# Optimization experiments

Measured on AMD Instinct MI355X. Metric: run time of the kernel, lower is better.

The kernel has to match this reference:

```python
import jax, jax.numpy as jnp
import numpy as np

N = 100000   # nodes
E = 1200000  # edges
D = 64       # emb_dim
XIN = 18     # x_dim + node_dim
XD = 16      # x_dim (output)
ED = 1       # edge_dim
L = 4        # num message-passing layers
G = 8        # graphs in batch (for global_mean_pool)


def setup_inputs() -> dict:
    key = jax.random.key(0)
    ks = iter(jax.random.split(key, 64))
    def nrm(shape, s=0.05):
        return jax.random.normal(next(ks), shape, dtype=jnp.float32) * s
    inp = {}
    inp["x"] = jax.random.normal(next(ks), (N, XIN), dtype=jnp.float32)
    inp["edge_attr"] = jax.random.normal(next(ks), (E, ED), dtype=jnp.float32)
    inp["W_in"] = nrm((XIN, D)); inp["b_in"] = jnp.zeros((D,), jnp.float32)
    # per-layer stacked params (leading dim L)
    inp["msg_W1"] = nrm((L, 2 * D + ED, D)); inp["msg_b1"] = jnp.zeros((L, D), jnp.float32)
    inp["msg_g1"] = jnp.ones((L, D), jnp.float32); inp["msg_be1"] = jnp.zeros((L, D), jnp.float32)
    inp["msg_W2"] = nrm((L, D, D)); inp["msg_b2"] = jnp.zeros((L, D), jnp.float32)
    inp["msg_g2"] = jnp.ones((L, D), jnp.float32); inp["msg_be2"] = jnp.zeros((L, D), jnp.float32)
    inp["upd_W1"] = nrm((L, 2 * D, D)); inp["upd_b1"] = jnp.zeros((L, D), jnp.float32)
    inp["upd_g1"] = jnp.ones((L, D), jnp.float32); inp["upd_be1"] = jnp.zeros((L, D), jnp.float32)
    inp["upd_W2"] = nrm((L, D, D)); inp["upd_b2"] = jnp.zeros((L, D), jnp.float32)
    inp["upd_g2"] = jnp.ones((L, D), jnp.float32); inp["upd_be2"] = jnp.zeros((L, D), jnp.float32)
    inp["reward_W"] = nrm((D, D)); inp["reward_b"] = jnp.zeros((D,), jnp.float32)
    inp["rout_W"] = nrm((D, 1)); inp["rout_b"] = jnp.zeros((1,), jnp.float32)
    inp["pred_W"] = nrm((D, D)); inp["pred_b"] = jnp.zeros((D,), jnp.float32)
    inp["pout_W"] = nrm((D, XD)); inp["pout_b"] = jnp.zeros((XD,), jnp.float32)
    inp["edge_index"] = jax.random.randint(next(ks), (2, E), 0, N)
    inp["batch"] = jnp.sort(jax.random.randint(next(ks), (N,), 0, G))
    return inp


def _bn(x, g, b, eps=1e-5):
    # BatchNorm1d in training mode: batch mean + biased variance
    m = jnp.mean(x, axis=0)
    v = jnp.mean((x - m) ** 2, axis=0)
    return (x - m) * jax.lax.rsqrt(v + eps) * g + b


def _mlp(x, W1, b1, g1, be1, W2, b2, g2, be2):
    h = jax.nn.relu(_bn(x @ W1 + b1, g1, be1))
    return jax.nn.relu(_bn(h @ W2 + b2, g2, be2))


def _forward(x, edge_attr, W_in, b_in,
             msg_W1, msg_b1, msg_g1, msg_be1, msg_W2, msg_b2, msg_g2, msg_be2,
             upd_W1, upd_b1, upd_g1, upd_be1, upd_W2, upd_b2, upd_g2, upd_be2,
             reward_W, reward_b, rout_W, rout_b, pred_W, pred_b, pout_W, pout_b,
             edge_index, batch):
    src = edge_index[0]  # j (source)
    dst = edge_index[1]  # i (target); PyG default flow source_to_target
    n = x.shape[0]
    h = x @ W_in + b_in
    for l in range(L):
        # message: gather + concat + MLP(psi)
        m = jnp.concatenate([h[dst], h[src], edge_attr], axis=-1)  # (E, 2D+ED)
        m = _mlp(m, msg_W1[l], msg_b1[l], msg_g1[l], msg_be1[l],
                 msg_W2[l], msg_b2[l], msg_g2[l], msg_be2[l])
        # aggregate: scatter-add to target nodes
        agg = jax.ops.segment_sum(m, dst, num_segments=n)  # (N, D)
        # update: concat + MLP(phi); residual add from outer network
        u = jnp.concatenate([h, agg], axis=-1)
        h = h + _mlp(u, upd_W1[l], upd_b1[l], upd_g1[l], upd_be1[l],
                     upd_W2[l], upd_b2[l], upd_g2[l], upd_be2[l])
    # reward head (computed in the original forward but not returned)
    h_reward = h @ reward_W + reward_b
    cnt = jax.ops.segment_sum(jnp.ones((n,), h.dtype), batch, num_segments=G)
    h_graph = jax.ops.segment_sum(h_reward, batch, num_segments=G) / jnp.maximum(cnt, 1.0)[:, None]
    _out_reward = h_graph @ rout_W + rout_b  # unused, matches original return
    # prediction head
    x_out = jax.nn.relu(h @ pred_W + pred_b) @ pout_W + pout_b  # (N, XD)
    return x_out


def reference(x, edge_attr, W_in, b_in,
              msg_W1, msg_b1, msg_g1, msg_be1, msg_W2, msg_b2, msg_g2, msg_be2,
              upd_W1, upd_b1, upd_g1, upd_be1, upd_W2, upd_b2, upd_g2, upd_be2,
              reward_W, reward_b, rout_W, rout_b, pred_W, pred_b, pout_W, pout_b,
              edge_index, batch):
    return _forward(x, edge_attr, W_in, b_in,
                    msg_W1, msg_b1, msg_g1, msg_be1, msg_W2, msg_b2, msg_g2, msg_be2,
                    upd_W1, upd_b1, upd_g1, upd_be1, upd_W2, upd_b2, upd_g2, upd_be2,
                    reward_W, reward_b, rout_W, rout_b, pred_W, pred_b, pout_W, pout_b,
                    edge_index, batch)
```

## Files before the change

kernel.cpp:

```cpp
#include <hip/hip_runtime.h>
#include <hip/hip_fp16.h>

typedef unsigned short u16;
typedef unsigned int u32;
typedef __attribute__((ext_vector_type(8))) unsigned short us8;
typedef __attribute__((ext_vector_type(8))) _Float16 f16x8;
typedef __attribute__((ext_vector_type(4))) float f32x4;

#define EPS 1e-5f

__device__ __forceinline__ float h2f(u16 h){ __half v; *(u16*)&v = h; return __half2float(v); }
__device__ __forceinline__ u16 f2h(float f){ __half v = __float2half(f); return *(u16*)&v; }
__device__ __forceinline__ u32 pkh(float a, float b){ return (u32)f2h(a) | ((u32)f2h(b) << 16); }

__global__ __launch_bounds__(256) void k_in(const float* __restrict__ x,
    const float* __restrict__ Win, const float* __restrict__ bin,
    float* __restrict__ h, int N){
  __shared__ float Ws[18][64];
  __shared__ float xs[64][20];
  int tid = threadIdx.x;
  for (int i = tid; i < 18*64; i += 256) Ws[i>>6][i&63] = Win[i];
  int row0 = blockIdx.x * 64;
  for (int i = tid; i < 64*18; i += 256){
    int r = i/18, k = i - r*18;
    int row = row0 + r;
    xs[r][k] = (row < N) ? x[(size_t)row*18 + k] : 0.f;
  }
  __syncthreads();
  int rq = tid >> 4, dq = tid & 15;
  float4 b4 = *(const float4*)(bin + dq*4);
  float acc[4][4];
  #pragma unroll
  for (int j=0;j<4;j++){ acc[j][0]=b4.x; acc[j][1]=b4.y; acc[j][2]=b4.z; acc[j][3]=b4.w; }
  for (int k=0;k<18;k++){
    float4 wv = *(const float4*)&Ws[k][dq*4];
    #pragma unroll
    for (int j=0;j<4;j++){
      float v = xs[rq*4+j][k];
      acc[j][0]+=v*wv.x; acc[j][1]+=v*wv.y; acc[j][2]+=v*wv.z; acc[j][3]+=v*wv.w;
    }
  }
  #pragma unroll
  for (int j=0;j<4;j++){
    int row = row0 + rq*4 + j;
    if (row < N)
      *(float4*)(h + (size_t)row*64 + dq*4) = make_float4(acc[j][0],acc[j][1],acc[j][2],acc[j][3]);
  }
}

__global__ __launch_bounds__(256) void k_pq(const float* __restrict__ h,
    const float* __restrict__ A, const float* __restrict__ B,
    u16* __restrict__ P, u16* __restrict__ Q, int N){
  __shared__ float hs[64][68];
  __shared__ float As[64][64];
  __shared__ float Bs[64][64];
  int tid = threadIdx.x;
  for (int i = tid; i < 4096; i += 256){ As[i>>6][i&63] = A[i]; Bs[i>>6][i&63] = B[i]; }
  int row0 = blockIdx.x*64;
  for (int i = tid; i < 4096; i += 256){
    int r = i>>6, k = i&63; int row = row0+r;
    hs[r][k] = (row<N)? h[(size_t)row*64+k] : 0.f;
  }
  __syncthreads();
  int rq = tid>>4, dq = tid&15;
  float ap[4][4]={}, aq[4][4]={};
  for (int k=0;k<64;k+=4){
    float4 hv[4];
    #pragma unroll
    for (int j=0;j<4;j++) hv[j] = *(const float4*)&hs[rq*4+j][k];
    #pragma unroll
    for (int kk=0;kk<4;kk++){
      float4 av = *(const float4*)&As[k+kk][dq*4];
      float4 bv = *(const float4*)&Bs[k+kk][dq*4];
      #pragma unroll
      for (int j=0;j<4;j++){
        float v = ((const float*)&hv[j])[kk];
        ap[j][0]+=v*av.x; ap[j][1]+=v*av.y; ap[j][2]+=v*av.z; ap[j][3]+=v*av.w;
        aq[j][0]+=v*bv.x; aq[j][1]+=v*bv.y; aq[j][2]+=v*bv.z; aq[j][3]+=v*bv.w;
      }
    }
  }
  #pragma unroll
  for (int j=0;j<4;j++){
    int row = row0 + rq*4 + j;
    if (row<N){
      ushort4 pk, qk;
      pk.x=f2h(ap[j][0]); pk.y=f2h(ap[j][1]); pk.z=f2h(ap[j][2]); pk.w=f2h(ap[j][3]);
      qk.x=f2h(aq[j][0]); qk.y=f2h(aq[j][1]); qk.z=f2h(aq[j][2]); qk.w=f2h(aq[j][3]);
      *(ushort4*)(P+(size_t)row*64+dq*4) = pk;
      *(ushort4*)(Q+(size_t)row*64+dq*4) = qk;
    }
  }
}

__global__ __launch_bounds__(256) void k_hist(const int* __restrict__ ei, int* __restrict__ cnt, int E){
  int e = blockIdx.x*256 + threadIdx.x;
  if (e < E) atomicAdd(&cnt[ei[E+e]], 1);
}

__global__ __launch_bounds__(256) void k_scan_a(const int* __restrict__ cnt, int* __restrict__ rp,
    int* __restrict__ bsum, int N){
  __shared__ int sm[256];
  int tid = threadIdx.x;
  int i0 = blockIdx.x*1024 + tid*4;
  int v0 = (i0+0<N)? cnt[i0+0]:0;
  int v1 = (i0+1<N)? cnt[i0+1]:0;
  int v2 = (i0+2<N)? cnt[i0+2]:0;
  int v3 = (i0+3<N)? cnt[i0+3]:0;
  int s = v0+v1+v2+v3;
  sm[tid] = s; __syncthreads();
  for (int ofs=1; ofs<256; ofs<<=1){
    int v = sm[tid];
    if (tid >= ofs) v += sm[tid-ofs];
    __syncthreads(); sm[tid] = v; __syncthreads();
  }
  int base = sm[tid] - s;
  int a0 = base+v0, a1 = a0+v1, a2 = a1+v2, a3 = a2+v3;
  if (i0+0<N) rp[i0+0]=a0;
  if (i0+1<N) rp[i0+1]=a1;
  if (i0+2<N) rp[i0+2]=a2;
  if (i0+3<N) rp[i0+3]=a3;
  if (tid==255) bsum[blockIdx.x] = sm[255];
}

__global__ void k_scan_b(int* __restrict__ bsum, int NB){
  if (threadIdx.x==0){
    int run = 0;
    for (int b=0;b<NB;b++){ int t = bsum[b]; bsum[b] = run; run += t; }
  }
}

__global__ __launch_bounds__(256) void k_scan_c(const int* __restrict__ cnt, int* __restrict__ rp,
    int* __restrict__ wr, const int* __restrict__ bsum, int N, int E){
  int tid = threadIdx.x;
  int i0 = blockIdx.x*1024 + tid*4;
  int off = bsum[blockIdx.x];
  #pragma unroll
  for (int j=0;j<4;j++){
    int i = i0+j;
    if (i<N){ int ex = off + rp[i] - cnt[i]; rp[i] = ex; wr[i] = ex; }
  }
  if (blockIdx.x==0 && tid==0) rp[N] = E;
}

__global__ __launch_bounds__(256) void k_perm(const int* __restrict__ ei, const float* __restrict__ ea,
    int* __restrict__ wr, int2* __restrict__ seS, int E){
  int e = blockIdx.x*256 + threadIdx.x;
  if (e < E){
    int dn = ei[E+e];
    int pos = atomicAdd(&wr[dn], 1);
    seS[pos] = make_int2(ei[e], __float_as_int(ea[e]));
  }
}

__global__ __launch_bounds__(256) void k_t1s(const u16* __restrict__ P, const u16* __restrict__ Q,
    const int2* __restrict__ seS, const int* __restrict__ rp,
    const float* __restrict__ c1, const float* __restrict__ b1,
    u16* __restrict__ t, float* __restrict__ stats, int N){
  int tid = threadIdx.x;
  int lane = tid & 63, w = tid >> 6;
  int sub = lane >> 5;
  int dl = (lane & 31) * 2;
  float cv0 = c1[dl], cv1 = c1[dl+1];
  float bv0 = b1[dl], bv1 = b1[dl+1];
  float s0 = 0.f, s1 = 0.f, qs0 = 0.f, qs1 = 0.f;
  for (int n = blockIdx.x*4 + w; n < N; n += gridDim.x*4){
    int a = rp[n], b = rp[n+1];
    u32 pp = *(const u32*)(P + (size_t)n*64 + dl);
    float p0 = h2f((u16)(pp & 0xffffu)) + bv0;
    float p1 = h2f((u16)(pp >> 16)) + bv1;
    int p = a + sub;
    for (; p + 2 < b; p += 4){
      int2 seA = seS[p];
      int2 seB = seS[p+2];
      u32 qA = *(const u32*)(Q + (size_t)seA.x*64 + dl);
      u32 qB = *(const u32*)(Q + (size_t)seB.x*64 + dl);
      float eaA = __int_as_float(seA.y), eaB = __int_as_float(seB.y);
      float tA0 = p0 + h2f((u16)(qA & 0xffffu)) + eaA*cv0;
      float tA1 = p1 + h2f((u16)(qA >> 16)) + eaA*cv1;
      float tB0 = p0 + h2f((u16)(qB & 0xffffu)) + eaB*cv0;
      float tB1 = p1 + h2f((u16)(qB >> 16)) + eaB*cv1;
      *(u32*)(t + (size_t)p*64 + dl) = (u32)f2h(tA0) | ((u32)f2h(tA1) << 16);
      *(u32*)(t + (size_t)(p+2)*64 + dl) = (u32)f2h(tB0) | ((u32)f2h(tB1) << 16);
      s0 += tA0 + tB0; s1 += tA1 + tB1;
      qs0 += tA0*tA0 + tB0*tB0; qs1 += tA1*tA1 + tB1*tB1;
    }
    for (; p < b; p += 2){
      int2 se = seS[p];
      u32 qq = *(const u32*)(Q + (size_t)se.x*64 + dl);
      float ea = __int_as_float(se.y);
      float t0 = p0 + h2f((u16)(qq & 0xffffu)) + ea*cv0;
      float t1 = p1 + h2f((u16)(qq >> 16)) + ea*cv1;
      *(u32*)(t + (size_t)p*64 + dl) = (u32)f2h(t0) | ((u32)f2h(t1) << 16);
      s0 += t0; s1 += t1; qs0 += t0*t0; qs1 += t1*t1;
    }
  }
  __shared__ float sS[8][64], qS[8][64];
  int idx = w*2 + sub;
  sS[idx][dl] = s0; sS[idx][dl+1] = s1;
  qS[idx][dl] = qs0; qS[idx][dl+1] = qs1;
  __syncthreads();
  if (tid < 64){
    float ts = 0.f, tq = 0.f;
    #pragma unroll
    for (int r=0;r<8;r++){ ts += sS[r][tid]; tq += qS[r][tid]; }
    atomicAdd(&stats[tid], ts);
    atomicAdd(&stats[64+tid], tq);
  }
}

__global__ __launch_bounds__(256) void k_m2s(u16* __restrict__ t,
    const float* __restrict__ g1, const float* __restrict__ be1, const float* __restrict__ stats1,
    const float* __restrict__ W2, const float* __restrict__ b2,
    float* __restrict__ stats2, int E, float invE){
  __shared__ _Float16 yL[128][72];
  __shared__ _Float16 wL[64][72];
  __shared__ float scS[64], shS[64], b2S[64];
  int tid = threadIdx.x;
  if (tid < 64){
    float m = stats1[tid]*invE;
    float v = stats1[64+tid]*invE - m*m;
    float sc = g1[tid]*rsqrtf(v + EPS);
    scS[tid] = sc; shS[tid] = be1[tid] - m*sc;
    b2S[tid] = b2[tid];
  }
  for (int i = tid; i < 4096; i += 256){
    int k = i >> 6, n = i & 63;
    wL[n][k] = (_Float16)W2[i];
  }
  __syncthreads();
  int lane = tid & 63, wv = tid >> 6;
  int arow = lane & 15;
  int kgrp = lane >> 4;
  int srow = tid >> 1, sc0 = (tid & 1)*32;
  float bb[4][4];
  #pragma unroll
  for (int c=0;c<4;c++){
    #pragma unroll
    for (int r=0;r<4;r++) bb[c][r] = b2S[16*c + 4*kgrp + r];
  }
  float ssum[4][4] = {}, ssq[4][4] = {};
  int ntiles = (E + 127) >> 7;
  f16x8 ra, rb, rc, rd;
  {
    f16x8 z;
    #pragma unroll
    for (int j=0;j<8;j++) z[j] = (_Float16)0.f;
    ra = rb = rc = rd = z;
    int tile = blockIdx.x;
    int p = tile*128 + srow;
    if (tile < ntiles && p < E){
      const u16* src = t + (size_t)p*64 + sc0;
      ra = *(const f16x8*)(src);
      rb = *(const f16x8*)(src + 8);
      rc = *(const f16x8*)(src + 16);
      rd = *(const f16x8*)(src + 24);
    }
  }
  for (int tile = blockIdx.x; tile < ntiles; tile += gridDim.x){
    int e0 = tile << 7;
    {
      f16x8 v;
      #pragma unroll
      for (int j=0;j<8;j++){ int dd = sc0 + j;      v[j] = (_Float16)fmaxf((float)ra[j]*scS[dd] + shS[dd], 0.f); }
      *(f16x8*)&yL[srow][sc0]      = v;
      #pragma unroll
      for (int j=0;j<8;j++){ int dd = sc0 + 8 + j;  v[j] = (_Float16)fmaxf((float)rb[j]*scS[dd] + shS[dd], 0.f); }
      *(f16x8*)&yL[srow][sc0 + 8]  = v;
      #pragma unroll
      for (int j=0;j<8;j++){ int dd = sc0 + 16 + j; v[j] = (_Float16)fmaxf((float)rc[j]*scS[dd] + shS[dd], 0.f); }
      *(f16x8*)&yL[srow][sc0 + 16] = v;
      #pragma unroll
      for (int j=0;j<8;j++){ int dd = sc0 + 24 + j; v[j] = (_Float16)fmaxf((float)rd[j]*scS[dd] + shS[dd], 0.f); }
      *(f16x8*)&yL[srow][sc0 + 24] = v;
    }
    {
      int nt = tile + gridDim.x;
      if (nt < ntiles){
        int p = nt*128 + srow;
        if (p < E){
          const u16* src = t + (size_t)p*64 + sc0;
          ra = *(const f16x8*)(src);
          rb = *(const f16x8*)(src + 8);
          rc = *(const f16x8*)(src + 16);
          rd = *(const f16x8*)(src + 24);
        } else {
          f16x8 z;
          #pragma unroll
          for (int j=0;j<8;j++) z[j] = (_Float16)0.f;
          ra = rb = rc = rd = z;
        }
      }
    }
    __syncthreads();
    #pragma unroll
    for (int mf=0; mf<2; mf++){
      int row = 32*wv + 16*mf + arow;
      f16x8 y0 = *(const f16x8*)&yL[row][8*kgrp];
      f16x8 y1 = *(const f16x8*)&yL[row][32 + 8*kgrp];
      int e = e0 + 32*wv + 16*mf + arow;
      #pragma unroll
      for (int c=0;c<4;c++){
        f16x8 w0 = *(const f16x8*)&wL[16*c + arow][8*kgrp];
        f16x8 w1 = *(const f16x8*)&wL[16*c + arow][32 + 8*kgrp];
        f32x4 d = {0.f,0.f,0.f,0.f};
        d = __builtin_amdgcn_mfma_f32_16x16x32_f16(w0, y0, d, 0, 0, 0);
        d = __builtin_amdgcn_mfma_f32_16x16x32_f16(w1, y1, d, 0, 0, 0);
        if (e < E){
          float v0 = d[0] + bb[c][0];
          float v1 = d[1] + bb[c][1];
          float v2 = d[2] + bb[c][2];
          float v3 = d[3] + bb[c][3];
          ushort4 st;
          st.x = f2h(v0); st.y = f2h(v1); st.z = f2h(v2); st.w = f2h(v3);
          *(ushort4*)(t + (size_t)e*64 + 16*c + 4*kgrp) = st;
          ssum[c][0]+=v0; ssum[c][1]+=v1; ssum[c][2]+=v2; ssum[c][3]+=v3;
          ssq[c][0]+=v0*v0; ssq[c][1]+=v1*v1; ssq[c][2]+=v2*v2; ssq[c][3]+=v3*v3;
        }
      }
    }
    __syncthreads();
  }
  float* red = (float*)yL;
  int slot = wv*16 + arow;
  #pragma unroll
  for (int c=0;c<4;c++){
    #pragma unroll
    for (int r=0;r<4;r++)
      red[(16*c + 4*kgrp + r)*64 + slot] = ssum[c][r];
  }
  __syncthreads();
  if (tid < 64){
    float s = 0.f;
    for (int g=0; g<64; g++) s += red[tid*64 + g];
    atomicAdd(&stats2[tid], s);
  }
  __syncthreads();
  #pragma unroll
  for (int c=0;c<4;c++){
    #pragma unroll
    for (int r=0;r<4;r++)
      red[(16*c + 4*kgrp + r)*64 + slot] = ssq[c][r];
  }
  __syncthreads();
  if (tid < 64){
    float s = 0.f;
    for (int g=0; g<64; g++) s += red[tid*64 + g];
    atomicAdd(&stats2[64+tid], s);
  }
}

__global__ __launch_bounds__(256) void k_agg(const u16* __restrict__ t2, const int* __restrict__ rp,
    const float* __restrict__ g2, const float* __restrict__ be2, const float* __restrict__ stats2,
    float* __restrict__ agg, int N, float invE){
  __shared__ float scS[64], shS[64];
  int tid = threadIdx.x;
  if (tid < 64){
    float m = stats2[tid]*invE;
    float v = stats2[64+tid]*invE - m*m;
    float sc = g2[tid]*rsqrtf(v+EPS);
    scS[tid] = sc; shS[tid] = be2[tid] - m*sc;
  }
  __syncthreads();
  int lane = tid & 63, w = tid >> 6;
  int sub = lane >> 5;
  int dl = (lane & 31) * 2;
  float sc0 = scS[dl], sc1 = scS[dl+1], sh0 = shS[dl], sh1 = shS[dl+1];
  for (int n = blockIdx.x*4 + w; n < N; n += gridDim.x*4){
    int a = rp[n], b = rp[n+1];
    float a0 = 0.f, a1 = 0.f;
    int p = a + sub;
    for (; p + 2 < b; p += 4){
      u32 vA = *(const u32*)(t2 + (size_t)p*64 + dl);
      u32 vB = *(const u32*)(t2 + (size_t)(p+2)*64 + dl);
      a0 += fmaxf(h2f((u16)(vA & 0xffffu))*sc0 + sh0, 0.f)
          + fmaxf(h2f((u16)(vB & 0xffffu))*sc0 + sh0, 0.f);
      a1 += fmaxf(h2f((u16)(vA >> 16))*sc1 + sh1, 0.f)
          + fmaxf(h2f((u16)(vB >> 16))*sc1 + sh1, 0.f);
    }
    for (; p < b; p += 2){
      u32 vA = *(const u32*)(t2 + (size_t)p*64 + dl);
      a0 += fmaxf(h2f((u16)(vA & 0xffffu))*sc0 + sh0, 0.f);
      a1 += fmaxf(h2f((u16)(vA >> 16))*sc1 + sh1, 0.f);
    }
    a0 += __shfl_xor(a0, 32);
    a1 += __shfl_xor(a1, 32);
    if (sub == 0)
      *(float2*)(agg + (size_t)n*64 + dl) = make_float2(a0, a1);
  }
}

__global__ __launch_bounds__(256) void k_s1(const u16* __restrict__ P, const u16* __restrict__ Q,
    const float* __restrict__ ea, const int* __restrict__ ei,
    const float* __restrict__ c1, const float* __restrict__ b1,
    float* __restrict__ stats, int E){
  int tid = threadIdx.x;
  int d = tid & 63, w = tid >> 6;
  float cv = c1[d], bv = b1[d];
  float s = 0.f, sq = 0.f;
  for (int e = blockIdx.x*4 + w; e < E; e += gridDim.x*4){
    int dn = ei[E+e], sn = ei[e];
    float t = h2f(P[(size_t)dn*64+d]) + h2f(Q[(size_t)sn*64+d]) + ea[e]*cv + bv;
    s += t; sq += t*t;
  }
  __shared__ float sS[4][64], qS[4][64];
  sS[w][d] = s; qS[w][d] = sq;
  __syncthreads();
  if (tid < 64){
    float ts = sS[0][tid]+sS[1][tid]+sS[2][tid]+sS[3][tid];
    float tq = qS[0][tid]+qS[1][tid]+qS[2][tid]+qS[3][tid];
    atomicAdd(&stats[tid], ts);
    atomicAdd(&stats[64+tid], tq);
  }
}

__global__ __launch_bounds__(256) void k_m2b(const u16* __restrict__ P, const u16* __restrict__ Q,
    const float* __restrict__ ea, const int* __restrict__ ei,
    const float* __restrict__ c1, const float* __restrict__ b1,
    const float* __restrict__ g1, const float* __restrict__ be1,
    const float* __restrict__ stats1,
    const float* __restrict__ W2, const float* __restrict__ b2,
    float* __restrict__ stats2, int E, float invE){
  __shared__ float ys[64][68];
  __shared__ float Ws[64][64];
  __shared__ float scS[64], c1S[64], bS[64], b2S[64];
  int tid = threadIdx.x;
  if (tid < 64){
    float m = stats1[tid]*invE;
    float v = stats1[64+tid]*invE - m*m;
    float sc = g1[tid]*rsqrtf(v + EPS);
    float sh = be1[tid] - m*sc;
    scS[tid] = sc;
    c1S[tid] = c1[tid]*sc;
    bS[tid]  = b1[tid]*sc + sh;
    b2S[tid] = b2[tid];
  }
  for (int i=tid;i<4096;i+=256) Ws[i>>6][i&63] = W2[i];
  __syncthreads();
  int rq = tid>>4, dq = tid&15;
  float ssum[4]={}, ssq[4]={};
  int ntiles = (E+63)>>6;
  for (int tile = blockIdx.x; tile < ntiles; tile += gridDim.x){
    int e0 = tile<<6;
    for (int i = tid; i < 4096; i += 256){
      int el = i>>6, dd = i&63;
      int e = e0 + el;
      float y = 0.f;
      if (e < E){
        int dn = ei[E+e], sn = ei[e];
        float t = (h2f(P[(size_t)dn*64+dd]) + h2f(Q[(size_t)sn*64+dd]))*scS[dd] + ea[e]*c1S[dd] + bS[dd];
        y = fmaxf(t, 0.f);
      }
      ys[el][dd] = y;
    }
    __syncthreads();
    float acc[4][4];
    float4 b4 = *(const float4*)&b2S[dq*4];
    #pragma unroll
    for (int j=0;j<4;j++){ acc[j][0]=b4.x; acc[j][1]=b4.y; acc[j][2]=b4.z; acc[j][3]=b4.w; }
    for (int k=0;k<64;k+=4){
      float4 hv[4];
      #pragma unroll
      for (int j=0;j<4;j++) hv[j] = *(const float4*)&ys[rq*4+j][k];
      #pragma unroll
      for (int kk=0;kk<4;kk++){
        float4 wv = *(const float4*)&Ws[k+kk][dq*4];
        #pragma unroll
        for (int j=0;j<4;j++){
          float v = ((const float*)&hv[j])[kk];
          acc[j][0]+=v*wv.x; acc[j][1]+=v*wv.y; acc[j][2]+=v*wv.z; acc[j][3]+=v*wv.w;
        }
      }
    }
    #pragma unroll
    for (int j=0;j<4;j++){
      int e = e0 + rq*4 + j;
      if (e < E){
        #pragma unroll
        for (int c=0;c<4;c++){ float v=acc[j][c]; ssum[c]+=v; ssq[c]+=v*v; }
      }
    }
    __syncthreads();
  }
  float* red = &ys[0][0];
  #pragma unroll
  for (int c=0;c<4;c++) red[rq*64 + dq*4 + c] = ssum[c];
  __syncthreads();
  if (tid < 64){
    float t=0.f;
    for (int r=0;r<16;r++) t += red[r*64+tid];
    atomicAdd(&stats2[tid], t);
  }
  __syncthreads();
  #pragma unroll
  for (int c=0;c<4;c++) red[rq*64 + dq*4 + c] = ssq[c];
  __syncthreads();
  if (tid < 64){
    float t=0.f;
    for (int r=0;r<16;r++) t += red[r*64+tid];
    atomicAdd(&stats2[64+tid], t);
  }
}

__global__ __launch_bounds__(256) void k_sc_rec(const u16* __restrict__ P, const u16* __restrict__ Q,
    const float* __restrict__ ea, const int* __restrict__ ei,
    const float* __restrict__ c1, const float* __restrict__ b1,
    const float* __restrict__ g1, const float* __restrict__ be1, const float* __restrict__ stats1,
    const float* __restrict__ W2, const float* __restrict__ b2,
    const float* __restrict__ g2, const float* __restrict__ be2, const float* __restrict__ stats2,
    float* __restrict__ agg, int E, float invE){
  __shared__ float ys[64][68];
  __shared__ float Ws[64][64];
  __shared__ float scS[64], c1S[64], bS[64];
  __shared__ float s2S[64], h2S[64], b2S[64];
  int tid = threadIdx.x;
  if (tid < 64){
    float m = stats1[tid]*invE;
    float v = stats1[64+tid]*invE - m*m;
    float sc = g1[tid]*rsqrtf(v + EPS);
    scS[tid] = sc;
    c1S[tid] = c1[tid]*sc;
    bS[tid]  = b1[tid]*sc + be1[tid] - m*sc;
    float m2 = stats2[tid]*invE;
    float v2 = stats2[64+tid]*invE - m2*m2;
    float sc2 = g2[tid]*rsqrtf(v2+EPS);
    s2S[tid] = sc2; h2S[tid] = be2[tid] - m2*sc2;
    b2S[tid] = b2[tid];
  }
  for (int i=tid;i<4096;i+=256) Ws[i>>6][i&63] = W2[i];
  __syncthreads();
  int rq = tid>>4, dq = tid&15;
  int ntiles = (E+63)>>6;
  for (int tile = blockIdx.x; tile < ntiles; tile += gridDim.x){
    int e0 = tile<<6;
    for (int i = tid; i < 4096; i += 256){
      int el = i>>6, dd = i&63;
      int e = e0 + el;
      float y = 0.f;
      if (e < E){
        int dn = ei[E+e], sn = ei[e];
        float t = (h2f(P[(size_t)dn*64+dd]) + h2f(Q[(size_t)sn*64+dd]))*scS[dd] + ea[e]*c1S[dd] + bS[dd];
        y = fmaxf(t, 0.f);
      }
      ys[el][dd] = y;
    }
    __syncthreads();
    float acc[4][4];
    float4 b4 = *(const float4*)&b2S[dq*4];
    #pragma unroll
    for (int j=0;j<4;j++){ acc[j][0]=b4.x; acc[j][1]=b4.y; acc[j][2]=b4.z; acc[j][3]=b4.w; }
    for (int k=0;k<64;k+=4){
      float4 hv[4];
      #pragma unroll
      for (int j=0;j<4;j++) hv[j] = *(const float4*)&ys[rq*4+j][k];
      #pragma unroll
      for (int kk=0;kk<4;kk++){
        float4 wv = *(const float4*)&Ws[k+kk][dq*4];
        #pragma unroll
        for (int j=0;j<4;j++){
          float v = ((const float*)&hv[j])[kk];
          acc[j][0]+=v*wv.x; acc[j][1]+=v*wv.y; acc[j][2]+=v*wv.z; acc[j][3]+=v*wv.w;
        }
      }
    }
    float4 sc4 = *(const float4*)&s2S[dq*4];
    float4 sh4 = *(const float4*)&h2S[dq*4];
    #pragma unroll
    for (int j=0;j<4;j++){
      int e = e0 + rq*4 + j;
      if (e < E){
        int dn = ei[E+e];
        float y0 = fmaxf(acc[j][0]*sc4.x + sh4.x, 0.f);
        float y1 = fmaxf(acc[j][1]*sc4.y + sh4.y, 0.f);
        float y2 = fmaxf(acc[j][2]*sc4.z + sh4.z, 0.f);
        float y3 = fmaxf(acc[j][3]*sc4.w + sh4.w, 0.f);
        atomicAdd(&agg[(size_t)dn*64 + dq*4    ], y0);
        atomicAdd(&agg[(size_t)dn*64 + dq*4 + 1], y1);
        atomicAdd(&agg[(size_t)dn*64 + dq*4 + 2], y2);
        atomicAdd(&agg[(size_t)dn*64 + dq*4 + 3], y3);
      }
    }
    __syncthreads();
  }
}

__global__ __launch_bounds__(256) void k_up1(const float* __restrict__ h, const float* __restrict__ agg,
    const float* __restrict__ U1, const float* __restrict__ b1u,
    float* __restrict__ tn, float* __restrict__ stats3, int N){
  __shared__ _Float16 yL[64][136];
  __shared__ _Float16 wL[64][136];
  __shared__ float bS[64];
  int tid = threadIdx.x;
  if (tid < 64) bS[tid] = b1u[tid];
  for (int i = tid; i < 8192; i += 256){
    int k = i >> 6, n = i & 63;
    wL[n][k] = (_Float16)U1[i];
  }
  int row0 = blockIdx.x * 64;
  int srow = tid >> 2, sc0 = (tid & 3) * 16;
  {
    int row = row0 + srow;
    if (row < N){
      #pragma unroll
      for (int c=0;c<4;c++){
        float4 v = *(const float4*)(h + (size_t)row*64 + sc0 + 4*c);
        *(u32*)&yL[srow][sc0+4*c]   = pkh(v.x, v.y);
        *(u32*)&yL[srow][sc0+4*c+2] = pkh(v.z, v.w);
      }
      #pragma unroll
      for (int c=0;c<4;c++){
        float4 v = *(const float4*)(agg + (size_t)row*64 + sc0 + 4*c);
        *(u32*)&yL[srow][64+sc0+4*c]   = pkh(v.x, v.y);
        *(u32*)&yL[srow][64+sc0+4*c+2] = pkh(v.z, v.w);
      }
    } else {
      #pragma unroll
      for (int c=0;c<4;c++){
        *(u32*)&yL[srow][sc0+4*c] = 0u; *(u32*)&yL[srow][sc0+4*c+2] = 0u;
        *(u32*)&yL[srow][64+sc0+4*c] = 0u; *(u32*)&yL[srow][64+sc0+4*c+2] = 0u;
      }
    }
  }
  __syncthreads();
  int lane = tid & 63, wv = tid >> 6;
  int arow = lane & 15, kgrp = lane >> 4;
  f16x8 a[4];
  #pragma unroll
  for (int kk=0;kk<4;kk++) a[kk] = *(const f16x8*)&yL[16*wv + arow][32*kk + 8*kgrp];
  float ssum[4]={}, ssq[4]={};
  #pragma unroll
  for (int c=0;c<4;c++){
    f32x4 d = {0.f,0.f,0.f,0.f};
    #pragma unroll
    for (int kk=0;kk<4;kk++){
      f16x8 b = *(const f16x8*)&wL[16*c + arow][32*kk + 8*kgrp];
      d = __builtin_amdgcn_mfma_f32_16x16x32_f16(a[kk], b, d, 0, 0, 0);
    }
    int col = 16*c + arow;
    float bb = bS[col];
    #pragma unroll
    for (int r=0;r<4;r++){
      int row = row0 + 16*wv + 4*kgrp + r;
      if (row < N){
        float v = d[r] + bb;
        tn[(size_t)row*64 + col] = v;
        ssum[c]+=v; ssq[c]+=v*v;
      }
    }
  }
  __syncthreads();
  float* red = (float*)yL;
  #pragma unroll
  for (int c=0;c<4;c++) red[c*256 + tid] = ssum[c];
  __syncthreads();
  if (tid < 64){
    int cc = tid >> 4;
    float s = 0.f;
    for (int g=0; g<16; g++) s += red[cc*256 + g*16 + (tid & 15)];
    atomicAdd(&stats3[tid], s);
  }
  __syncthreads();
  #pragma unroll
  for (int c=0;c<4;c++) red[c*256 + tid] = ssq[c];
  __syncthreads();
  if (tid < 64){
    int cc = tid >> 4;
    float s = 0.f;
    for (int g=0; g<16; g++) s += red[cc*256 + g*16 + (tid & 15)];
    atomicAdd(&stats3[64+tid], s);
  }
}

__global__ __launch_bounds__(256) void k_up2(float* __restrict__ tn,
    const float* __restrict__ g3, const float* __restrict__ be3, const float* __restrict__ stats3,
    const float* __restrict__ U2, const float* __restrict__ b2u,
    float* __restrict__ stats4, int N, float invN){
  __shared__ _Float16 yL[64][72];
  __shared__ _Float16 wL[64][72];
  __shared__ float scS[64], shS[64], bS[64];
  int tid = threadIdx.x;
  if (tid < 64){
    float m = stats3[tid]*invN;
    float v = stats3[64+tid]*invN - m*m;
    float sc = g3[tid]*rsqrtf(v+EPS);
    scS[tid] = sc; shS[tid] = be3[tid] - m*sc; bS[tid] = b2u[tid];
  }
  for (int i = tid; i < 4096; i += 256){
    int k = i >> 6, n = i & 63;
    wL[n][k] = (_Float16)U2[i];
  }
  __syncthreads();
  int row0 = blockIdx.x * 64;
  int srow = tid >> 2, sc0 = (tid & 3) * 16;
  {
    int row = row0 + srow;
    if (row < N){
      #pragma unroll
      for (int c=0;c<4;c++){
        float4 v = *(const float4*)(tn + (size_t)row*64 + sc0 + 4*c);
        int d0 = sc0 + 4*c;
        float y0 = fmaxf(v.x*scS[d0  ] + shS[d0  ], 0.f);
        float y1 = fmaxf(v.y*scS[d0+1] + shS[d0+1], 0.f);
        float y2 = fmaxf(v.z*scS[d0+2] + shS[d0+2], 0.f);
        float y3 = fmaxf(v.w*scS[d0+3] + shS[d0+3], 0.f);
        *(u32*)&yL[srow][d0]   = pkh(y0, y1);
        *(u32*)&yL[srow][d0+2] = pkh(y2, y3);
      }
    } else {
      #pragma unroll
      for (int c=0;c<4;c++){
        *(u32*)&yL[srow][sc0+4*c] = 0u; *(u32*)&yL[srow][sc0+4*c+2] = 0u;
      }
    }
  }
  __syncthreads();
  int lane = tid & 63, wv = tid >> 6;
  int arow = lane & 15, kgrp = lane >> 4;
  f16x8 a0 = *(const f16x8*)&yL[16*wv + arow][8*kgrp];
  f16x8 a1 = *(const f16x8*)&yL[16*wv + arow][32 + 8*kgrp];
  float ssum[4]={}, ssq[4]={};
  #pragma unroll
  for (int c=0;c<4;c++){
    f16x8 b0 = *(const f16x8*)&wL[16*c + arow][8*kgrp];
    f16x8 b1 = *(const f16x8*)&wL[16*c + arow][32 + 8*kgrp];
    f32x4 d = {0.f,0.f,0.f,0.f};
    d = __builtin_amdgcn_mfma_f32_16x16x32_f16(a0, b0, d, 0, 0, 0);
    d = __builtin_amdgcn_mfma_f32_16x16x32_f16(a1, b1, d, 0, 0, 0);
    int col = 16*c + arow;
    float bb = bS[col];
    #pragma unroll
    for (int r=0;r<4;r++){
      int row = row0 + 16*wv + 4*kgrp + r;
      if (row < N){
        float v = d[r] + bb;
        tn[(size_t)row*64 + col] = v;
        ssum[c]+=v; ssq[c]+=v*v;
      }
    }
  }
  __syncthreads();
  float* red = (float*)yL;
  #pragma unroll
  for (int c=0;c<4;c++) red[c*256 + tid] = ssum[c];
  __syncthreads();
  if (tid < 64){
    int cc = tid >> 4;
    float s = 0.f;
    for (int g=0; g<16; g++) s += red[cc*256 + g*16 + (tid & 15)];
    atomicAdd(&stats4[tid], s);
  }
  __syncthreads();
  #pragma unroll
  for (int c=0;c<4;c++) red[c*256 + tid] = ssq[c];
  __syncthreads();
  if (tid < 64){
    int cc = tid >> 4;
    float s = 0.f;
    for (int g=0; g<16; g++) s += red[cc*256 + g*16 + (tid & 15)];
    atomicAdd(&stats4[64+tid], s);
  }
}

__global__ __launch_bounds__(256) void k_res_pq(float* __restrict__ h, const float* __restrict__ tn,
    const float* __restrict__ g4, const float* __restrict__ be4, const float* __restrict__ stats4,
    const float* __restrict__ A, const float* __restrict__ B,
    u16* __restrict__ P, u16* __restrict__ Q, int N, float invN){
  __shared__ _Float16 yL[64][72];
  __shared__ _Float16 wLa[64][72];
  __shared__ _Float16 wLb[64][72];
  __shared__ float scS[64], shS[64];
  int tid = threadIdx.x;
  if (tid < 64){
    float m = stats4[tid]*invN;
    float v = stats4[64+tid]*invN - m*m;
    float sc = g4[tid]*rsqrtf(v+EPS);
    scS[tid] = sc; shS[tid] = be4[tid] - m*sc;
  }
  for (int i = tid; i < 4096; i += 256){
    int k = i >> 6, n = i & 63;
    wLa[n][k] = (_Float16)A[i];
    wLb[n][k] = (_Float16)B[i];
  }
  __syncthreads();
  int row0 = blockIdx.x * 64;
  int srow = tid >> 2, sc0 = (tid & 3) * 16;
  {
    int row = row0 + srow;
    if (row < N){
      #pragma unroll
      for (int c=0;c<4;c++){
        int d0 = sc0 + 4*c;
        float4 hv4 = *(const float4*)(h + (size_t)row*64 + d0);
        float4 tv4 = *(const float4*)(tn + (size_t)row*64 + d0);
        float h0 = hv4.x + fmaxf(tv4.x*scS[d0  ] + shS[d0  ], 0.f);
        float h1 = hv4.y + fmaxf(tv4.y*scS[d0+1] + shS[d0+1], 0.f);
        float h2 = hv4.z + fmaxf(tv4.z*scS[d0+2] + shS[d0+2], 0.f);
        float h3 = hv4.w + fmaxf(tv4.w*scS[d0+3] + shS[d0+3], 0.f);
        *(float4*)(h + (size_t)row*64 + d0) = make_float4(h0,h1,h2,h3);
        *(u32*)&yL[srow][d0]   = pkh(h0, h1);
        *(u32*)&yL[srow][d0+2] = pkh(h2, h3);
      }
    } else {
      #pragma unroll
      for (int c=0;c<4;c++){
        *(u32*)&yL[srow][sc0+4*c] = 0u; *(u32*)&yL[srow][sc0+4*c+2] = 0u;
      }
    }
  }
  __syncthreads();
  int lane = tid & 63, wv = tid >> 6;
  int arow = lane & 15, kgrp = lane >> 4;
  f16x8 y0 = *(const f16x8*)&yL[16*wv + arow][8*kgrp];
  f16x8 y1 = *(const f16x8*)&yL[16*wv + arow][32 + 8*kgrp];
  int node = row0 + 16*wv + arow;
  #pragma unroll
  for (int c=0;c<4;c++){
    f16x8 wa0 = *(const f16x8*)&wLa[16*c + arow][8*kgrp];
    f16x8 wa1 = *(const f16x8*)&wLa[16*c + arow][32 + 8*kgrp];
    f32x4 dp = {0.f,0.f,0.f,0.f};
    dp = __builtin_amdgcn_mfma_f32_16x16x32_f16(wa0, y0, dp, 0, 0, 0);
    dp = __builtin_amdgcn_mfma_f32_16x16x32_f16(wa1, y1, dp, 0, 0, 0);
    f16x8 wb0 = *(const f16x8*)&wLb[16*c + arow][8*kgrp];
    f16x8 wb1 = *(const f16x8*)&wLb[16*c + arow][32 + 8*kgrp];
    f32x4 dq = {0.f,0.f,0.f,0.f};
    dq = __builtin_amdgcn_mfma_f32_16x16x32_f16(wb0, y0, dq, 0, 0, 0);
    dq = __builtin_amdgcn_mfma_f32_16x16x32_f16(wb1, y1, dq, 0, 0, 0);
    if (node < N){
      ushort4 pk4, qk4;
      pk4.x = f2h(dp[0]); pk4.y = f2h(dp[1]); pk4.z = f2h(dp[2]); pk4.w = f2h(dp[3]);
      qk4.x = f2h(dq[0]); qk4.y = f2h(dq[1]); qk4.z = f2h(dq[2]); qk4.w = f2h(dq[3]);
      *(ushort4*)(P + (size_t)node*64 + 16*c + 4*kgrp) = pk4;
      *(ushort4*)(Q + (size_t)node*64 + 16*c + 4*kgrp) = qk4;
    }
  }
}

__global__ __launch_bounds__(256) void k_res_head(const float* __restrict__ h, const float* __restrict__ tn,
    const float* __restrict__ g4, const float* __restrict__ be4, const float* __restrict__ stats4,
    const float* __restrict__ Wp, const float* __restrict__ bp,
    const float* __restrict__ Wo, const float* __restrict__ bo,
    float* __restrict__ out, int N, float invN){
  __shared__ float hs[64][68];
  __shared__ float Wps[64][64];
  __shared__ float ps[64][68];
  __shared__ float Wos[64][16];
  __shared__ float scS[64], shS[64];
  int tid = threadIdx.x;
  if (tid < 64){
    float m = stats4[tid]*invN;
    float v = stats4[64+tid]*invN - m*m;
    float sc = g4[tid]*rsqrtf(v+EPS);
    scS[tid] = sc; shS[tid] = be4[tid] - m*sc;
  }
  for (int i=tid;i<4096;i+=256) Wps[i>>6][i&63] = Wp[i];
  for (int i=tid;i<1024;i+=256) Wos[i>>4][i&15] = Wo[i];
  int row0 = blockIdx.x*64;
  __syncthreads();
  for (int i = tid; i < 4096; i += 256){
    int r = i>>6, k = i&63; int row = row0+r;
    float hv = 0.f;
    if (row<N)
      hv = h[(size_t)row*64+k] + fmaxf(tn[(size_t)row*64+k]*scS[k] + shS[k], 0.f);
    hs[r][k] = hv;
  }
  __syncthreads();
  int rq = tid>>4, dq = tid&15;
  float4 b4 = *(const float4*)(bp + dq*4);
  float acc[4][4];
  #pragma unroll
  for (int j=0;j<4;j++){ acc[j][0]=b4.x; acc[j][1]=b4.y; acc[j][2]=b4.z; acc[j][3]=b4.w; }
  for (int k=0;k<64;k+=4){
    float4 hv[4];
    #pragma unroll
    for (int j=0;j<4;j++) hv[j] = *(const float4*)&hs[rq*4+j][k];
    #pragma unroll
    for (int kk=0;kk<4;kk++){
      float4 wv = *(const float4*)&Wps[k+kk][dq*4];
      #pragma unroll
      for (int j=0;j<4;j++){
        float v = ((const float*)&hv[j])[kk];
        acc[j][0]+=v*wv.x; acc[j][1]+=v*wv.y; acc[j][2]+=v*wv.z; acc[j][3]+=v*wv.w;
      }
    }
  }
  #pragma unroll
  for (int j=0;j<4;j++){
    *(float4*)&ps[rq*4+j][dq*4] = make_float4(fmaxf(acc[j][0],0.f), fmaxf(acc[j][1],0.f),
                                              fmaxf(acc[j][2],0.f), fmaxf(acc[j][3],0.f));
  }
  __syncthreads();
  int f = tid & 15;
  float bof = bo[f];
  float acc2[4] = {bof, bof, bof, bof};
  for (int k=0;k<64;k++){
    float wv = Wos[k][f];
    #pragma unroll
    for (int j=0;j<4;j++) acc2[j] += ps[rq*4+j][k]*wv;
  }
  #pragma unroll
  for (int j=0;j<4;j++){
    int row = row0 + rq*4 + j;
    if (row<N) out[(size_t)row*16 + f] = acc2[j];
  }
}

extern "C" void kernel_launch(void* const* d_in, const int* in_sizes, int n_in,
                              void* d_out, int out_size, void* d_ws, size_t ws_size,
                              hipStream_t stream){
  const float* x    = (const float*)d_in[0];
  const float* eatt = (const float*)d_in[1];
  const float* Win  = (const float*)d_in[2];
  const float* bin  = (const float*)d_in[3];
  const float* mW1  = (const float*)d_in[4];
  const float* mb1  = (const float*)d_in[5];
  const float* mg1  = (const float*)d_in[6];
  const float* mbe1 = (const float*)d_in[7];
  const float* mW2  = (const float*)d_in[8];
  const float* mb2  = (const float*)d_in[9];
  const float* mg2  = (const float*)d_in[10];
  const float* mbe2 = (const float*)d_in[11];
  const float* uW1  = (const float*)d_in[12];
  const float* ub1  = (const float*)d_in[13];
  const float* ug1  = (const float*)d_in[14];
  const float* ube1 = (const float*)d_in[15];
  const float* uW2  = (const float*)d_in[16];
  const float* ub2  = (const float*)d_in[17];
  const float* ug2  = (const float*)d_in[18];
  const float* ube2 = (const float*)d_in[19];
  const float* predW = (const float*)d_in[24];
  const float* predb = (const float*)d_in[25];
  const float* poutW = (const float*)d_in[26];
  const float* poutb = (const float*)d_in[27];
  const int*   ei    = (const int*)d_in[28];

  const int N = in_sizes[0] / 18;
  const int E = in_sizes[1];

  size_t nodeB = (size_t)N * 64 * sizeof(float);
  size_t halfB = (size_t)N * 64 * sizeof(u16);
  size_t t2B   = (size_t)E * 64 * sizeof(u16);
  size_t statsB = 16 * 128 * sizeof(float);
  int NB = (N + 1023)/1024;
  size_t csrB = (size_t)E*8 + (size_t)(N+1)*4 + (size_t)N*4 + (size_t)N*4 + 4096*4;

  bool planA = ws_size >= nodeB + 2*halfB + nodeB + t2B + csrB + statsB;

  char* w = (char*)d_ws;
  float* h = (float*)w; w += nodeB;
  u16* P = (u16*)w; w += halfB;
  u16* Q = (u16*)w; w += halfB;
  float* agg = (float*)w; w += nodeB;
  float* tn = agg;
  u16*  t2 = nullptr;
  int2* seS = nullptr;
  int *rp=nullptr, *cnt=nullptr, *wrp=nullptr, *bsum=nullptr;
  float* stats;
  if (planA){
    t2   = (u16*)w;  w += t2B;
    seS  = (int2*)w; w += (size_t)E*8;
    rp   = (int*)w;  w += (size_t)(N+1)*4;
    cnt  = (int*)w;  w += (size_t)N*4;
    wrp  = (int*)w;  w += (size_t)N*4;
    bsum = (int*)w;  w += 4096*4;
    stats = (float*)w;
  } else {
    stats = (float*)w;
  }

  hipMemsetAsync(stats, 0, statsB, stream);

  int nb = (N + 63)/64;
  float invE = 1.0f/(float)E, invN = 1.0f/(float)N;

  k_in<<<nb, 256, 0, stream>>>(x, Win, bin, h, N);
  k_pq<<<nb, 256, 0, stream>>>(h, mW1, mW1 + 4096, P, Q, N);

  if (planA){
    hipMemsetAsync(cnt, 0, (size_t)N*4, stream);
    k_hist<<<(E+255)/256, 256, 0, stream>>>(ei, cnt, E);
    k_scan_a<<<NB, 256, 0, stream>>>(cnt, rp, bsum, N);
    k_scan_b<<<1, 64, 0, stream>>>(bsum, NB);
    k_scan_c<<<NB, 256, 0, stream>>>(cnt, rp, wrp, bsum, N, E);
    k_perm<<<(E+255)/256, 256, 0, stream>>>(ei, eatt, wrp, seS, E);
  }

  for (int l = 0; l < 4; ++l){
    float* s1 = stats + (l*4+0)*128;
    float* s2 = stats + (l*4+1)*128;
    float* s3 = stats + (l*4+2)*128;
    float* s4 = stats + (l*4+3)*128;
    const float* A  = mW1 + (size_t)l*8256;
    const float* c1 = A + 8192;
    if (planA){
      k_t1s<<<2048, 256, 0, stream>>>(P, Q, seS, rp, c1, mb1 + l*64, t2, s1, N);
      k_m2s<<<2048, 256, 0, stream>>>(t2, mg1 + l*64, mbe1 + l*64, s1,
                                      mW2 + (size_t)l*4096, mb2 + l*64, s2, E, invE);
      k_agg<<<2048, 256, 0, stream>>>(t2, rp, mg2 + l*64, mbe2 + l*64, s2, agg, N, invE);
    } else {
      k_s1<<<2048, 256, 0, stream>>>(P, Q, eatt, ei, c1, mb1 + l*64, s1, E);
      k_m2b<<<1024, 256, 0, stream>>>(P, Q, eatt, ei, c1, mb1 + l*64, mg1 + l*64, mbe1 + l*64,
                                      s1, mW2 + (size_t)l*4096, mb2 + l*64, s2, E, invE);
      hipMemsetAsync(agg, 0, nodeB, stream);
      k_sc_rec<<<1024, 256, 0, stream>>>(P, Q, eatt, ei, c1, mb1 + l*64, mg1 + l*64, mbe1 + l*64,
                                         s1, mW2 + (size_t)l*4096, mb2 + l*64,
                                         mg2 + l*64, mbe2 + l*64, s2, agg, E, invE);
    }
    k_up1<<<nb, 256, 0, stream>>>(h, agg, uW1 + (size_t)l*8192, ub1 + l*64, tn, s3, N);
    k_up2<<<nb, 256, 0, stream>>>(tn, ug1 + l*64, ube1 + l*64, s3, uW2 + (size_t)l*4096,
                                  ub2 + l*64, s4, N, invN);
    if (l < 3){
      const float* An = mW1 + (size_t)(l+1)*8256;
      k_res_pq<<<nb, 256, 0, stream>>>(h, tn, ug2 + l*64, ube2 + l*64, s4,
                                       An, An + 4096, P, Q, N, invN);
    } else {
      k_res_head<<<nb, 256, 0, stream>>>(h, tn, ug2 + l*64, ube2 + l*64, s4,
                                         predW, predb, poutW, poutb, (float*)d_out, N, invN);
    }
  }
}
```

Before: 1.854 ms.

## Fuse CSR aggregation into first update-MLP GEMM kernel

```diff
diff --git a/kernel.cpp b/kernel.cpp
--- a/kernel.cpp
+++ b/kernel.cpp
@@ -350,43 +350,123 @@
   }
 }
 
-__global__ __launch_bounds__(256) void k_agg(const u16* __restrict__ t2, const int* __restrict__ rp,
+__global__ __launch_bounds__(256) void k_aggup1(const float* __restrict__ h,
+    const u16* __restrict__ t2, const int* __restrict__ rp,
     const float* __restrict__ g2, const float* __restrict__ be2, const float* __restrict__ stats2,
-    float* __restrict__ agg, int N, float invE){
-  __shared__ float scS[64], shS[64];
+    const float* __restrict__ U1, const float* __restrict__ b1u,
+    float* __restrict__ tn, float* __restrict__ stats3, int N, float invE){
+  __shared__ _Float16 yL[64][136];
+  __shared__ _Float16 wL[64][136];
+  __shared__ float scS[64], shS[64], bS[64];
   int tid = threadIdx.x;
   if (tid < 64){
     float m = stats2[tid]*invE;
     float v = stats2[64+tid]*invE - m*m;
     float sc = g2[tid]*rsqrtf(v+EPS);
     scS[tid] = sc; shS[tid] = be2[tid] - m*sc;
-  }
-  __syncthreads();
-  int lane = tid & 63, w = tid >> 6;
-  int sub = lane >> 5;
-  int dl = (lane & 31) * 2;
-  float sc0 = scS[dl], sc1 = scS[dl+1], sh0 = shS[dl], sh1 = shS[dl+1];
-  for (int n = blockIdx.x*4 + w; n < N; n += gridDim.x*4){
-    int a = rp[n], b = rp[n+1];
-    float a0 = 0.f, a1 = 0.f;
-    int p = a + sub;
-    for (; p + 2 < b; p += 4){
-      u32 vA = *(const u32*)(t2 + (size_t)p*64 + dl);
-      u32 vB = *(const u32*)(t2 + (size_t)(p+2)*64 + dl);
-      a0 += fmaxf(h2f((u16)(vA & 0xffffu))*sc0 + sh0, 0.f)
-          + fmaxf(h2f((u16)(vB & 0xffffu))*sc0 + sh0, 0.f);
-      a1 += fmaxf(h2f((u16)(vA >> 16))*sc1 + sh1, 0.f)
-          + fmaxf(h2f((u16)(vB >> 16))*sc1 + sh1, 0.f);
-    }
-    for (; p < b; p += 2){
-      u32 vA = *(const u32*)(t2 + (size_t)p*64 + dl);
-      a0 += fmaxf(h2f((u16)(vA & 0xffffu))*sc0 + sh0, 0.f);
-      a1 += fmaxf(h2f((u16)(vA >> 16))*sc1 + sh1, 0.f);
-    }
-    a0 += __shfl_xor(a0, 32);
-    a1 += __shfl_xor(a1, 32);
-    if (sub == 0)
-      *(float2*)(agg + (size_t)n*64 + dl) = make_float2(a0, a1);
+    bS[tid] = b1u[tid];
+  }
+  for (int i = tid; i < 8192; i += 256){
+    int k = i >> 6, n = i & 63;
+    wL[n][k] = (_Float16)U1[i];
+  }
+  int row0 = blockIdx.x * 64;
+  int srow = tid >> 2, sc0 = (tid & 3) * 16;
+  {
+    int row = row0 + srow;
+    if (row < N){
+      #pragma unroll
+      for (int c=0;c<4;c++){
+        float4 v = *(const float4*)(h + (size_t)row*64 + sc0 + 4*c);
+        *(u32*)&yL[srow][sc0+4*c]   = pkh(v.x, v.y);
+        *(u32*)&yL[srow][sc0+4*c+2] = pkh(v.z, v.w);
+      }
+    } else {
+      #pragma unroll
+      for (int c=0;c<4;c++){
+        *(u32*)&yL[srow][sc0+4*c] = 0u; *(u32*)&yL[srow][sc0+4*c+2] = 0u;
+      }
+    }
+  }
+  __syncthreads();
+  {
+    int lane = tid & 63, w = tid >> 6;
+    int sub = lane >> 5;
+    int dl = (lane & 31) * 2;
+    float sc0f = scS[dl], sc1f = scS[dl+1], sh0 = shS[dl], sh1 = shS[dl+1];
+    for (int i=0;i<16;i++){
+      int n = row0 + w*16 + i;
+      float a0 = 0.f, a1 = 0.f;
+      if (n < N){
+        int a = rp[n], b = rp[n+1];
+        int p = a + sub;
+        for (; p + 2 < b; p += 4){
+          u32 vA = *(const u32*)(t2 + (size_t)p*64 + dl);
+          u32 vB = *(const u32*)(t2 + (size_t)(p+2)*64 + dl);
+          a0 += fmaxf(h2f((u16)(vA & 0xffffu))*sc0f + sh0, 0.f)
+              + fmaxf(h2f((u16)(vB & 0xffffu))*sc0f + sh0, 0.f);
+          a1 += fmaxf(h2f((u16)(vA >> 16))*sc1f + sh1, 0.f)
+              + fmaxf(h2f((u16)(vB >> 16))*sc1f + sh1, 0.f);
+        }
+        for (; p < b; p += 2){
+          u32 vA = *(const u32*)(t2 + (size_t)p*64 + dl);
+          a0 += fmaxf(h2f((u16)(vA & 0xffffu))*sc0f + sh0, 0.f);
+          a1 += fmaxf(h2f((u16)(vA >> 16))*sc1f + sh1, 0.f);
+        }
+      }
+      a0 += __shfl_xor(a0, 32);
+      a1 += __shfl_xor(a1, 32);
+      if (sub == 0)
+        *(u32*)&yL[w*16 + i][64 + dl] = pkh(a0, a1);
+    }
+  }
+  __syncthreads();
+  int lane = tid & 63, wv = tid >> 6;
+  int arow = lane & 15, kgrp = lane >> 4;
+  f16x8 a[4];
+  #pragma unroll
+  for (int kk=0;kk<4;kk++) a[kk] = *(const f16x8*)&yL[16*wv + arow][32*kk + 8*kgrp];
+  float ssum[4]={}, ssq[4]={};
+  #pragma unroll
+  for (int c=0;c<4;c++){
+    f32x4 d = {0.f,0.f,0.f,0.f};
+    #pragma unroll
+    for (int kk=0;kk<4;kk++){
+      f16x8 b = *(const f16x8*)&wL[16*c + arow][32*kk + 8*kgrp];
+      d = __builtin_amdgcn_mfma_f32_16x16x32_f16(a[kk], b, d, 0, 0, 0);
+    }
+    int col = 16*c + arow;
+    float bb = bS[col];
+    #pragma unroll
+    for (int r=0;r<4;r++){
+      int row = row0 + 16*wv + 4*kgrp + r;
+      if (row < N){
+        float v = d[r] + bb;
+        tn[(size_t)row*64 + col] = v;
+        ssum[c]+=v; ssq[c]+=v*v;
+      }
+    }
+  }
+  __syncthreads();
+  float* red = (float*)yL;
+  #pragma unroll
+  for (int c=0;c<4;c++) red[c*256 + tid] = ssum[c];
+  __syncthreads();
+  if (tid < 64){
+    int cc = tid >> 4;
+    float s = 0.f;
+    for (int g=0; g<16; g++) s += red[cc*256 + g*16 + (tid & 15)];
+    atomicAdd(&stats3[tid], s);
+  }
+  __syncthreads();
+  #pragma unroll
+  for (int c=0;c<4;c++) red[c*256 + tid] = ssq[c];
+  __syncthreads();
+  if (tid < 64){
+    int cc = tid >> 4;
+    float s = 0.f;
+    for (int g=0; g<16; g++) s += red[cc*256 + g*16 + (tid & 15)];
+    atomicAdd(&stats3[64+tid], s);
   }
 }
 
@@ -995,7 +1075,8 @@
       k_t1s<<<2048, 256, 0, stream>>>(P, Q, seS, rp, c1, mb1 + l*64, t2, s1, N);
       k_m2s<<<2048, 256, 0, stream>>>(t2, mg1 + l*64, mbe1 + l*64, s1,
                                       mW2 + (size_t)l*4096, mb2 + l*64, s2, E, invE);
-      k_agg<<<2048, 256, 0, stream>>>(t2, rp, mg2 + l*64, mbe2 + l*64, s2, agg, N, invE);
+      k_aggup1<<<nb, 256, 0, stream>>>(h, t2, rp, mg2 + l*64, mbe2 + l*64, s2,
+                                       uW1 + (size_t)l*8192, ub1 + l*64, tn, s3, N, invE);
     } else {
       k_s1<<<2048, 256, 0, stream>>>(P, Q, eatt, ei, c1, mb1 + l*64, s1, E);
       k_m2b<<<1024, 256, 0, stream>>>(P, Q, eatt, ei, c1, mb1 + l*64, mg1 + l*64, mbe1 + l*64,
@@ -1004,8 +1085,8 @@
       k_sc_rec<<<1024, 256, 0, stream>>>(P, Q, eatt, ei, c1, mb1 + l*64, mg1 + l*64, mbe1 + l*64,
                                          s1, mW2 + (size_t)l*4096, mb2 + l*64,
                                          mg2 + l*64, mbe2 + l*64, s2, agg, E, invE);
-    }
-    k_up1<<<nb, 256, 0, stream>>>(h, agg, uW1 + (size_t)l*8192, ub1 + l*64, tn, s3, N);
+      k_up1<<<nb, 256, 0, stream>>>(h, agg, uW1 + (size_t)l*8192, ub1 + l*64, tn, s3, N);
+    }
     k_up2<<<nb, 256, 0, stream>>>(tn, ug1 + l*64, ube1 + l*64, s3, uW2 + (size_t)l*4096,
                                   ub2 + l*64, s4, N, invN);
     if (l < 3){
```

New measurement: 1.926 ms. +3.8%, slower.
